# Kernel optimization log

Measured on AMD Instinct MI355X. Metric: run time of the kernel, lower is better.

The kernel has to match this reference:

```python
import jax, jax.numpy as jnp
import numpy as np


def setup_inputs() -> dict:
    key = jax.random.key(0)
    B, S, D = 8, 2048, 1024
    inputs = jax.random.normal(key, (B, S, D), dtype=jnp.float32)
    return {"inputs": inputs}


def reference(inputs):
    # scores = X X^T / seq_len  (source divides by dk = inputs.shape[-2], the seq dim)
    seq_len = inputs.shape[-2]
    scores = jnp.einsum('bsd,btd->bst', inputs, inputs) / seq_len
    scores = jax.nn.softmax(scores, axis=-1)
    # context is computed in the original but not returned; keep the matmul for fidelity
    context = jnp.einsum('bst,btd->bsd', scores, inputs)
    del context
    return (inputs, scores)
```

## Files before the change

### kernel.cpp

```cpp
#include <hip/hip_runtime.h>

typedef unsigned short ushort_t;
using short8 = __attribute__((ext_vector_type(8))) short;
using half4  = __attribute__((ext_vector_type(4))) _Float16;
using half8  = __attribute__((ext_vector_type(8))) _Float16;
using f32x4  = __attribute__((ext_vector_type(4))) float;

#define AS1 __attribute__((address_space(1)))
#define AS3 __attribute__((address_space(3)))

#define B_   8
#define S_   2048
#define D_   1024
#define NIN  (8UL * 2048UL * 1024UL)
#define PARTS 32
#define SROWB 8192UL
#define BATCHB (2048UL * SROWB)


__device__ __forceinline__ ushort_t f2bf(float f) {
    unsigned u = __float_as_uint(f);
    u += 0x7FFFu + ((u >> 16) & 1u);
    return (ushort_t)(u >> 16);
}

__global__ __launch_bounds__(256) void cvtcopy_packed(const float* __restrict__ in,
                                                      float* __restrict__ outcopy,
                                                      char* sc) {
    size_t g = ((size_t)blockIdx.x * 256 + threadIdx.x) * 8;
    const float4* p = (const float4*)(in + g);
    float4 a = p[0], c = p[1];
    float4* q = (float4*)(outcopy + g);
    q[0] = a; q[1] = c;
    short8 r;
    r[0] = (short)f2bf(a.x); r[1] = (short)f2bf(a.y);
    r[2] = (short)f2bf(a.z); r[3] = (short)f2bf(a.w);
    r[4] = (short)f2bf(c.x); r[5] = (short)f2bf(c.y);
    r[6] = (short)f2bf(c.z); r[7] = (short)f2bf(c.w);
    size_t xrow = g >> 10;
    size_t col  = g & 1023;
    char* dst = sc + xrow * SROWB + 2048 + col * 2;
    *(short8*)dst = r;
}

__global__ __launch_bounds__(256, 2) void gemm_sym2(char* sc) {
    __shared__ __align__(16) ushort_t sA[2][128 * 64];
    __shared__ __align__(16) ushort_t sB[2][128 * 64];

    const int lin = blockIdx.x;
    const int wg  = (lin & 7) * 136 + (lin >> 3);
    const int b   = wg / 136;
    int rem = wg % 136, ti = 0;
    while (rem >= 16 - ti) { rem -= 16 - ti; ++ti; }
    const int tj = ti + rem;
    const int tr = ti * 128, tc = tj * 128;

    char* Sb = sc + (size_t)b * BATCHB;

    const int tid  = threadIdx.x;
    const int lane = tid & 63;
    const int wid  = tid >> 6;
    const int wr = (wid >> 1) * 64;
    const int wc = (wid & 1) * 64;

    f32x4 acc[4][4] = {};

    const int srow_s = tid >> 3;
    const int cd     = tid & 7;
    const int rsel = lane & 15;
    const int g4   = lane >> 4;
    const int sw   = lane & 7;

    auto stage = [&](int s, int slot) {
#pragma unroll
        for (int j = 0; j < 4; ++j) {
            const int row = j * 32 + srow_s;
            const int csw = (cd ^ (row & 7)) << 4;
            const size_t rbA = (size_t)(tr + row) * SROWB + 2048 + (size_t)s * 128;
            const size_t rbB = (size_t)(tc + row) * SROWB + 2048 + (size_t)s * 128;
            __builtin_amdgcn_global_load_lds((const AS1 void*)(Sb + rbA + csw),
                (AS3 void*)((char*)&sA[slot][0] + j * 4096 + tid * 16), 16, 0, 0);
            __builtin_amdgcn_global_load_lds((const AS1 void*)(Sb + rbB + csw),
                (AS3 void*)((char*)&sB[slot][0] + j * 4096 + tid * 16), 16, 0, 0);
        }
    };

    stage(0, 0);
    stage(1, 1);
    asm volatile("s_waitcnt vmcnt(8)" ::: "memory");
    __builtin_amdgcn_s_barrier();

#pragma unroll
    for (int s = 0; s < 16; ++s) {
        const int slot = s & 1;

        short8 af[2][4], bfr[2][4];
#pragma unroll
        for (int kk = 0; kk < 2; ++kk) {
            const int cb = kk * 4 + g4;
            const int csw = (cb ^ sw) << 4;
#pragma unroll
            for (int m = 0; m < 4; ++m) {
                const int row = wr + m * 16 + rsel;
                af[kk][m] = *(const short8*)((const char*)&sA[slot][0] + row * 128 + csw);
            }
#pragma unroll
            for (int n = 0; n < 4; ++n) {
                const int row = wc + n * 16 + rsel;
                bfr[kk][n] = *(const short8*)((const char*)&sB[slot][0] + row * 128 + csw);
            }
        }
        asm volatile("s_waitcnt lgkmcnt(0)" ::: "memory");
        __builtin_amdgcn_s_barrier();

        if (s + 2 < 16) {
            stage(s + 2, slot);
            asm volatile("s_waitcnt vmcnt(8)" ::: "memory");
        } else if (s == 14) {
            asm volatile("s_waitcnt vmcnt(0)" ::: "memory");
        }
        __builtin_amdgcn_s_barrier();

        __builtin_amdgcn_s_setprio(1);
#pragma unroll
        for (int kk = 0; kk < 2; ++kk)
#pragma unroll
            for (int m = 0; m < 4; ++m)
#pragma unroll
                for (int n = 0; n < 4; ++n)
                    acc[m][n] = __builtin_amdgcn_mfma_f32_16x16x32_bf16(
                        af[kk][m], bfr[kk][n], acc[m][n], 0, 0, 0);
        __builtin_amdgcn_s_setprio(0);
    }

    const float scale = 1.0f / 2048.0f;
    const int r0 = (lane >> 4) * 4;
    const int c0 = lane & 15;

#pragma unroll
    for (int m = 0; m < 4; ++m)
#pragma unroll
        for (int n = 0; n < 4; ++n)
#pragma unroll
            for (int rr = 0; rr < 4; ++rr)
                acc[m][n][rr] = __expf(acc[m][n][rr] * scale);

#pragma unroll
    for (int m = 0; m < 4; ++m) {
#pragma unroll
        for (int n = 0; n < 4; ++n) {
            char* dbase = Sb + (size_t)(tr + wr + m * 16 + r0) * SROWB + 4096
                             + (size_t)(tc + wc + n * 16 + c0) * 2;
#pragma unroll
            for (int rr = 0; rr < 4; ++rr)
                *(_Float16*)(dbase + (size_t)rr * SROWB) = (_Float16)acc[m][n][rr];
        }
    }

#pragma unroll
    for (int m = 0; m < 4; ++m) {
#pragma unroll
        for (int rr = 0; rr < 4; ++rr) {
            float s = (acc[m][0][rr] + acc[m][1][rr]) + (acc[m][2][rr] + acc[m][3][rr]);
            s += __shfl_xor(s, 1, 64);
            s += __shfl_xor(s, 2, 64);
            s += __shfl_xor(s, 4, 64);
            s += __shfl_xor(s, 8, 64);
            if ((lane & 15) == 0) {
                char* prow = Sb + (size_t)(tr + wr + m * 16 + r0 + rr) * SROWB;
                ((float*)prow)[tj * 2 + (wid & 1)] = s;
            }
        }
    }

    if (ti != tj) {
#pragma unroll
        for (int m = 0; m < 4; ++m) {
#pragma unroll
            for (int n = 0; n < 4; ++n) {
                half4 h;
#pragma unroll
                for (int rr = 0; rr < 4; ++rr) h[rr] = (_Float16)acc[m][n][rr];
                char* mb = Sb + (size_t)(tc + wc + n * 16 + c0) * SROWB + 4096
                              + (size_t)(tr + wr + m * 16 + r0) * 2;
                *(half4*)mb = h;
            }
        }
#pragma unroll
        for (int n = 0; n < 4; ++n) {
            float s = 0.0f;
#pragma unroll
            for (int m = 0; m < 4; ++m)
#pragma unroll
                for (int rr = 0; rr < 4; ++rr) s += acc[m][n][rr];
            s += __shfl_xor(s, 16, 64);
            s += __shfl_xor(s, 32, 64);
            if (lane < 16) {
                char* prow = Sb + (size_t)(tc + wc + n * 16 + lane) * SROWB;
                ((float*)prow)[ti * 2 + (wid >> 1)] = s;
            }
        }
    }
}

__global__ __launch_bounds__(256) void normalize_rows(char* sc) {
    const int row  = blockIdx.x * 4 + (threadIdx.x >> 6);
    const int lane = threadIdx.x & 63;
    char* rowc = sc + (size_t)row * SROWB;
    const _Float16* e = (const _Float16*)(rowc + 4096);
    float* s = (float*)rowc;

    float p = (lane < PARTS) ? ((const float*)rowc)[lane] : 0.0f;
#pragma unroll
    for (int o = 32; o > 0; o >>= 1) p += __shfl_xor(p, o, 64);
    const float inv = 1.0f / p;

    half8 v[4];
#pragma unroll
    for (int c = 0; c < 4; ++c)
        v[c] = *(const half8*)(e + c * 512 + lane * 8);

#pragma unroll
    for (int c = 0; c < 4; ++c) {
        float4 f0, f1;
        f0.x = (float)v[c][0] * inv; f0.y = (float)v[c][1] * inv;
        f0.z = (float)v[c][2] * inv; f0.w = (float)v[c][3] * inv;
        f1.x = (float)v[c][4] * inv; f1.y = (float)v[c][5] * inv;
        f1.z = (float)v[c][6] * inv; f1.w = (float)v[c][7] * inv;
        *(float4*)(s + c * 512 + lane * 8)     = f0;
        *(float4*)(s + c * 512 + lane * 8 + 4) = f1;
    }
}

extern "C" void kernel_launch(void* const* d_in, const int* in_sizes, int n_in,
                              void* d_out, int out_size, void* d_ws, size_t ws_size,
                              hipStream_t stream) {
    const float* X = (const float*)d_in[0];
    float* out = (float*)d_out;
    char*  sc  = (char*)d_out + NIN * 4;

    cvtcopy_packed<<<NIN / (256 * 8), 256, 0, stream>>>(X, out, sc);
    gemm_sym2<<<1088, 256, 0, stream>>>(sc);
    normalize_rows<<<(B_ * S_) / 4, 256, 0, stream>>>(sc);
}
```

Measured before the change: 123.6 us.

## Move fp32 input copy from conversion kernel into GEMM main loop

The fp32 passthrough copy of the inputs no longer happens in the conversion kernel. The first 1024 GEMM workgroups now copy it in 16 chunks interleaved with the K loop, with per-iteration vmcnt waits adjusted for the extra in-flight loads and stores. The aim is to hide the 64MB copy's bandwidth under the compute-bound GEMM and shrink the memory-bound conversion kernel. In exchange, the GEMM's vector memory queue gets busier and the wait counts are hand-tuned, so an error there could cause stalls or races.

Result: faster. 118.8 us (-3.9%).

```diff
diff --git a/kernel.cpp b/kernel.cpp
--- a/kernel.cpp
+++ b/kernel.cpp
@@ -24,14 +24,11 @@
     return (ushort_t)(u >> 16);
 }
 
-__global__ __launch_bounds__(256) void cvtcopy_packed(const float* __restrict__ in,
-                                                      float* __restrict__ outcopy,
-                                                      char* sc) {
+__global__ __launch_bounds__(256) void cvt_packed(const float* __restrict__ in,
+                                                  char* sc) {
     size_t g = ((size_t)blockIdx.x * 256 + threadIdx.x) * 8;
     const float4* p = (const float4*)(in + g);
     float4 a = p[0], c = p[1];
-    float4* q = (float4*)(outcopy + g);
-    q[0] = a; q[1] = c;
     short8 r;
     r[0] = (short)f2bf(a.x); r[1] = (short)f2bf(a.y);
     r[2] = (short)f2bf(a.z); r[3] = (short)f2bf(a.w);
@@ -43,7 +40,9 @@
     *(short8*)dst = r;
 }
 
-__global__ __launch_bounds__(256, 2) void gemm_sym2(char* sc) {
+__global__ __launch_bounds__(256, 2) void gemm_sym3(char* sc,
+                                                    const float4* xin,
+                                                    float4* xout) {
     __shared__ __align__(16) ushort_t sA[2][128 * 64];
     __shared__ __align__(16) ushort_t sB[2][128 * 64];
 
@@ -63,7 +62,11 @@
     const int wr = (wid >> 1) * 64;
     const int wc = (wid & 1) * 64;
 
+    const bool docopy = (lin < 1024);
+    const size_t cbase = (size_t)lin * 256 + tid;
+
     f32x4 acc[4][4] = {};
+    float4 creg;
 
     const int srow_s = tid >> 3;
     const int cd     = tid & 7;
@@ -113,11 +116,21 @@
         asm volatile("s_waitcnt lgkmcnt(0)" ::: "memory");
         __builtin_amdgcn_s_barrier();
 
-        if (s + 2 < 16) {
-            stage(s + 2, slot);
-            asm volatile("s_waitcnt vmcnt(8)" ::: "memory");
-        } else if (s == 14) {
-            asm volatile("s_waitcnt vmcnt(0)" ::: "memory");
+        if (s + 2 < 16) stage(s + 2, slot);
+
+        if (docopy) {
+            if (s > 0) xout[cbase + (size_t)(s - 1) * 262144] = creg;
+            creg = xin[cbase + (size_t)s * 262144];
+        }
+
+        if (docopy) {
+            if (s == 0)       asm volatile("s_waitcnt vmcnt(9)"  ::: "memory");
+            else if (s == 1)  asm volatile("s_waitcnt vmcnt(11)" ::: "memory");
+            else if (s < 14)  asm volatile("s_waitcnt vmcnt(12)" ::: "memory");
+            else if (s == 14) asm volatile("s_waitcnt vmcnt(4)"  ::: "memory");
+        } else {
+            if (s + 2 < 16)   asm volatile("s_waitcnt vmcnt(8)"  ::: "memory");
+            else if (s == 14) asm volatile("s_waitcnt vmcnt(0)"  ::: "memory");
         }
         __builtin_amdgcn_s_barrier();
 
@@ -132,6 +145,8 @@
                         af[kk][m], bfr[kk][n], acc[m][n], 0, 0, 0);
         __builtin_amdgcn_s_setprio(0);
     }
+
+    if (docopy) xout[cbase + 15UL * 262144] = creg;
 
     const float scale = 1.0f / 2048.0f;
     const int r0 = (lane >> 4) * 4;
@@ -239,7 +254,7 @@
     float* out = (float*)d_out;
     char*  sc  = (char*)d_out + NIN * 4;
 
-    cvtcopy_packed<<<NIN / (256 * 8), 256, 0, stream>>>(X, out, sc);
-    gemm_sym2<<<1088, 256, 0, stream>>>(sc);
+    cvt_packed<<<NIN / (256 * 8), 256, 0, stream>>>(X, sc);
+    gemm_sym3<<<1088, 256, 0, stream>>>(sc, (const float4*)X, (float4*)out);
     normalize_rows<<<(B_ * S_) / 4, 256, 0, stream>>>(sc);
 }
```
